# Optimization experiments

Hardware: AMD Instinct MI355X
Metric: run time of the kernel (lower is better)

The kernel has to match this reference:

```python
import jax, jax.numpy as jnp
import numpy as np

N, C, D, S = 512, 128, 16, 10
IR_DIMS = (1, 3, 5, 7)      # 0e, 1o, 2e, 3o
MUL1, MUL2, MUL3 = 1, 3, 7  # symmetric tensor-product path counts per order
INV_SQRT_C = 1.0 / np.sqrt(C).astype(np.float32)


def setup_inputs() -> dict:
    key = jax.random.key(0)
    ks = jax.random.split(key, 20)
    inp = {
        "node_feats": jax.random.normal(ks[0], (N, C, D), jnp.float32),
        "node_specie": jax.random.randint(ks[1], (N,), 0, S, jnp.int32),
    }
    # U basis tensors (stand-ins for e3nn reduced symmetric tensor product basis):
    # shape (D,)*order + (num_paths, ir_dim)
    for i, di in enumerate(IR_DIMS):
        inp[f"u1_{i}"] = jax.random.normal(ks[2 + i], (D, MUL1, di), jnp.float32) * 0.1
        inp[f"u2_{i}"] = jax.random.normal(ks[6 + i], (D, D, MUL2, di), jnp.float32) * 0.1
        inp[f"u3_{i}"] = jax.random.normal(ks[10 + i], (D, D, D, MUL3, di), jnp.float32) * 0.1
    # species-conditioned weights, init stddev mul**-0.5 (gradient_normalization='element')
    inp["w1"] = jax.random.normal(ks[14], (4, S, MUL1, C), jnp.float32) * MUL1 ** -0.5
    inp["w2"] = jax.random.normal(ks[15], (4, S, MUL2, C), jnp.float32) * MUL2 ** -0.5
    inp["w3"] = jax.random.normal(ks[16], (4, S, MUL3, C), jnp.float32) * MUL3 ** -0.5
    # e3nn Linear weights per output irrep: (C_in, C_out)
    inp["wlin"] = jax.random.normal(ks[17], (4, C, C), jnp.float32)
    return inp


def _product_basis(x, node_specie, u1s, u2s, u3s, w1, w2, w3, wlin):
    # x: (N, C, D). Recursive MACE symmetric contraction, vectorized over nodes.
    outs = []
    for i in range(4):  # loop over the 4 output irreps (fixed, structurally distinct)
        w3i = w3[i][node_specie]  # (N, MUL3, C) species gather
        w2i = w2[i][node_specie]  # (N, MUL2, C)
        w1i = w1[i][node_specie]  # (N, MUL1, C)
        # order 3: einsum('abjki,kc,cj->cabi', u3, w, x) per node
        a = jnp.einsum('nkc,ncj->njkc', w3i, x)               # (N, D, MUL3, C)
        out = jnp.einsum('abjki,njkc->ncabi', u3s[i], a)      # (N, C, D, D, di)
        # order 2 contribution, then contract one feature axis with x
        out = out + jnp.einsum('abki,nkc->ncabi', u2s[i], w2i)
        out = jnp.einsum('ncaji,ncj->ncai', out, x)           # (N, C, D, di)
        # order 1 contribution, then final contraction with x
        out = out + jnp.einsum('aki,nkc->ncai', u1s[i], w1i)
        out = jnp.einsum('ncji,ncj->nci', out, x)             # (N, C, di)
        # axis_to_mul + e3nn Linear (channel mixing per irrep, 1/sqrt(fan_in))
        y = jnp.einsum('nci,cf->nfi', out, wlin[i]) * INV_SQRT_C
        outs.append(y.reshape(y.shape[0], -1))
    return jnp.concatenate(outs, axis=-1)  # (N, C * sum(IR_DIMS)) = (N, 2048)


def reference(node_feats, node_specie, u1_0, u1_1, u1_2, u1_3,
              u2_0, u2_1, u2_2, u2_3, u3_0, u3_1, u3_2, u3_3,
              w1, w2, w3, wlin):
    return _product_basis(node_feats, node_specie,
                          (u1_0, u1_1, u1_2, u1_3),
                          (u2_0, u2_1, u2_2, u2_3),
                          (u3_0, u3_1, u3_2, u3_3),
                          w1, w2, w3, wlin)
```

## Files before the change

### kernel.cpp

```cpp
#include <hip/hip_runtime.h>

#define N_NODES 512
#define C_CH    128
#define S_SPEC  10
#define KT      50
#define NT      11

typedef _Float16 h8 __attribute__((ext_vector_type(8)));
typedef float f32x4 __attribute__((ext_vector_type(4)));

__device__ h8 g_Bf[KT * NT * 64];
__device__ h8 g_Wf[128 * 64];

__device__ __forceinline__ void o_to_iri(int o, int& ir, int& i) {
  if (o >= 9)      { ir = 3; i = o - 9; }
  else if (o >= 4) { ir = 2; i = o - 4; }
  else if (o >= 1) { ir = 1; i = o - 1; }
  else             { ir = 0; i = 0; }
}

__device__ int octet_desc(int Q) {
  if (Q < 172) {
    int q = Q;
    for (int a = 0; a < 16; ++a)
      for (int b = a; b < 16; ++b) {
        int no = (b < 8) ? 2 : 1;
        if (q < no) {
          int jb = (no == 1) ? 1 : q;
          return a | (b << 5) | (jb << 10);
        }
        q -= no;
      }
  } else if (Q < 196) {
    int q = Q - 172;
    for (int a = 0; a < 16; ++a) {
      int no = (a < 8) ? 2 : 1;
      if (q < no) {
        int jb = (no == 1) ? 1 : q;
        return a | (16 << 5) | (jb << 10);
      }
      q -= no;
    }
  } else if (Q < 198) {
    return 16 | (16 << 5) | ((Q - 196) << 10);
  }
  return 17 | (17 << 5);
}

__global__ void build_all(const float* __restrict__ u1_0, const float* __restrict__ u1_1,
                          const float* __restrict__ u1_2, const float* __restrict__ u1_3,
                          const float* __restrict__ u2_0, const float* __restrict__ u2_1,
                          const float* __restrict__ u2_2, const float* __restrict__ u2_3,
                          const float* __restrict__ u3_0, const float* __restrict__ u3_1,
                          const float* __restrict__ u3_2, const float* __restrict__ u3_3,
                          const float* __restrict__ wlin) {
  const int bid = blockIdx.x;
  const int dis[4] = {1, 3, 5, 7};
  if (bid < 320) {
    int kt, nt;
    if (bid < 301)      { kt = bid / 7; nt = bid % 7; }
    else if (bid < 319) { int e = bid - 301; kt = 43 + e / 3; nt = 7 + e % 3; }
    else                { kt = 49; nt = 10; }

    const int l = threadIdx.x;
    const int o = l & 15;
    int ir, ii; o_to_iri(o, ir, ii);
    const int di = dis[ir];
    const float* u1s[4] = {u1_0, u1_1, u1_2, u1_3};
    const float* u2s[4] = {u2_0, u2_1, u2_2, u2_3};
    const float* u3s[4] = {u3_0, u3_1, u3_2, u3_3};

    const int rt = octet_desc(kt * 4 + (l >> 4));
    const int oA = rt & 31, oB = (rt >> 5) & 31, j0 = ((rt >> 10) & 1) * 8;

    h8 v;
#pragma unroll
    for (int i = 0; i < 8; ++i) {
      const int j = j0 + i;
      float val = 0.f;
      if (oA < 16 && oB < 16) {
        if (j >= oB) {
          const float* u = u3s[ir];
          int a = oA, b = oB;
          int P[6][3] = {{a,b,j},{a,j,b},{b,a,j},{b,j,a},{j,a,b},{j,b,a}};
          for (int p = 0; p < 6; ++p) {
            bool dup = false;
            for (int r = 0; r < p; ++r)
              if (P[r][0] == P[p][0] && P[r][1] == P[p][1] && P[r][2] == P[p][2]) { dup = true; break; }
            if (!dup)
              val += u[(((P[p][0] * 16 + P[p][1]) * 16 + P[p][2]) * 7 + nt) * di + ii];
          }
        }
      } else if (oA < 16 && oB == 16) {
        if (j >= oA) {
          const int k2 = nt - 7;
          const float* u = u2s[ir];
          val = u[((oA * 16 + j) * 3 + k2) * di + ii];
          if (j != oA) val += u[((j * 16 + oA) * 3 + k2) * di + ii];
        }
      } else if (oA == 16) {
        val = u1s[ir][j * di + ii];
      }
      v[i] = (_Float16)val;
    }
    g_Bf[((size_t)kt * NT + nt) * 64 + l] = v;
  } else {
    const int id = (bid - 320) * 64 + threadIdx.x;
    const int l = id & 63, ks = (id >> 6) & 15, mt = id >> 10;
    const int f = mt * 16 + (l & 15);
    const float inv = 0.08838834764831845f;
    h8 v;
#pragma unroll
    for (int i = 0; i < 8; ++i) {
      const int k = ks * 32 + (l >> 4) * 8 + i;
      const int ir = k >> 7, cc = k & 127;
      v[i] = (_Float16)(wlin[((size_t)ir * C_CH + cc) * C_CH + f] * inv);
    }
    g_Wf[(mt * 16 + ks) * 64 + l] = v;
  }
}


#define MFMA16(A, B, C) __builtin_amdgcn_mfma_f32_16x16x32_f16(A, B, C, 0, 0, 0)

__global__ __launch_bounds__(512, 1) void eqp_mm(
    const float* __restrict__ x, const int* __restrict__ specie,
    const float* __restrict__ w1, const float* __restrict__ w2,
    const float* __restrict__ w3, float* __restrict__ out) {
  __shared__ __align__(16) char bs[2][70 * 1024];
  __shared__ float xT[2][128][18];
  __shared__ int rtab[KT * 4];

  const int t = threadIdx.x;
  const int l = t & 63;
  const int w = t >> 6;
  const int g = l >> 4;
  const int n0 = blockIdx.x * 2;

  {
    const int p = t >> 8, c = (t >> 1) & 127, half = t & 1;
    const float* xp = x + ((size_t)(n0 + p) * C_CH + c) * 16 + half * 8;
    const float4 v0 = *(const float4*)xp, v1 = *(const float4*)(xp + 4);
    float* row = &xT[p][c][half * 8];
    row[0] = v0.x; row[1] = v0.y; row[2] = v0.z; row[3] = v0.w;
    row[4] = v1.x; row[5] = v1.y; row[6] = v1.z; row[7] = v1.w;
    if (half == 1) { xT[p][c][16] = 1.f; xT[p][c][17] = 0.f; }
    if (t < KT * 4) rtab[t] = octet_desc(t);
  }

  const int ch = w * 16 + (l & 15);
  const int s0 = specie[n0], s1 = specie[n0 + 1];

  auto packh = [](float4 u, float4 v) {
    h8 r;
    r[0] = (_Float16)u.x; r[1] = (_Float16)u.y; r[2] = (_Float16)u.z; r[3] = (_Float16)u.w;
    r[4] = (_Float16)v.x; r[5] = (_Float16)v.y; r[6] = (_Float16)v.z; r[7] = (_Float16)v.w;
    return r;
  };
  h8 xh0l, xh0h, xh1l, xh1h;
  {
    const float4* p0 = (const float4*)(x + ((size_t)n0 * C_CH + ch) * 16);
    xh0l = packh(p0[0], p0[1]); xh0h = packh(p0[2], p0[3]);
    const float4* p1 = (const float4*)(x + ((size_t)(n0 + 1) * C_CH + ch) * 16);
    xh1l = packh(p1[0], p1[1]); xh1h = packh(p1[2], p1[3]);
  }

  f32x4 acc[2][NT];
#pragma unroll
  for (int p = 0; p < 2; ++p)
#pragma unroll
    for (int i = 0; i < NT; ++i) acc[p][i] = (f32x4){0.f, 0.f, 0.f, 0.f};

  h8 tv[9]; int dst[9];

  auto issue = [&](int ck) {
    const int f0 = ck * 70;
    const int nf = (ck < 4) ? 70 : 40;
#pragma unroll
    for (int slot = 0; slot < 9; ++slot) {
      const int r = slot * 8 + w;
      const bool ok = r < nf;
      const int fi = f0 + r;
      int kt, nt;
      if (fi < 301)      { kt = fi / 7;  nt = fi % 7; }
      else if (fi < 319) { kt = 43 + (fi - 301) / 3; nt = 7 + (fi - 301) % 3; }
      else               { kt = 49; nt = 10; }
      dst[slot] = ok ? r : -1;
      if (ok) tv[slot] = g_Bf[((size_t)kt * NT + nt) * 64 + l];
    }
  };
  auto wr = [&](char* buf) {
#pragma unroll
    for (int slot = 0; slot < 9; ++slot)
      if (dst[slot] >= 0) *(h8*)&buf[(size_t)dst[slot] * 1024 + (size_t)l * 16] = tv[slot];
  };

#define BRD(i) (*(const h8*)&buf[(size_t)(fb2 + (i)) * 1024 + (size_t)l * 16])

  auto consume = [&](int ck, const char* buf) {
    const int cs = ck * 10;
    int fb2 = 0;
#pragma unroll
    for (int tt = 0; tt < 10; ++tt) {
      const int kt = cs + tt;
      const int rt_ = rtab[kt * 4 + g];
      const int oA_ = rt_ & 31, oB_ = (rt_ >> 5) & 31, jb_ = (rt_ >> 10) & 1;
      const float xab0 = xT[0][ch][oA_] * xT[0][ch][oB_];
      const float xab1 = xT[1][ch][oA_] * xT[1][ch][oB_];
      const _Float16 hm0 = (_Float16)xab0, hm1 = (_Float16)xab1;
      const h8 m0 = {hm0, hm0, hm0, hm0, hm0, hm0, hm0, hm0};
      const h8 m1 = {hm1, hm1, hm1, hm1, hm1, hm1, hm1, hm1};
      const h8 af0 = m0 * (jb_ ? xh0h : xh0l);
      const h8 af1 = m1 * (jb_ ? xh1h : xh1l);
      if (kt < 43) {
        h8 b0 = BRD(0), b1 = BRD(1), b2 = BRD(2), b3 = BRD(3), b4 = BRD(4), b5 = BRD(5), b6 = BRD(6);
        acc[0][0] = MFMA16(af0, b0, acc[0][0]); acc[1][0] = MFMA16(af1, b0, acc[1][0]);
        acc[0][1] = MFMA16(af0, b1, acc[0][1]); acc[1][1] = MFMA16(af1, b1, acc[1][1]);
        acc[0][2] = MFMA16(af0, b2, acc[0][2]); acc[1][2] = MFMA16(af1, b2, acc[1][2]);
        acc[0][3] = MFMA16(af0, b3, acc[0][3]); acc[1][3] = MFMA16(af1, b3, acc[1][3]);
        acc[0][4] = MFMA16(af0, b4, acc[0][4]); acc[1][4] = MFMA16(af1, b4, acc[1][4]);
        acc[0][5] = MFMA16(af0, b5, acc[0][5]); acc[1][5] = MFMA16(af1, b5, acc[1][5]);
        acc[0][6] = MFMA16(af0, b6, acc[0][6]); acc[1][6] = MFMA16(af1, b6, acc[1][6]);
        fb2 += 7;
      } else if (kt < 49) {
        h8 b0 = BRD(0), b1 = BRD(1), b2 = BRD(2);
        acc[0][7] = MFMA16(af0, b0, acc[0][7]); acc[1][7] = MFMA16(af1, b0, acc[1][7]);
        acc[0][8] = MFMA16(af0, b1, acc[0][8]); acc[1][8] = MFMA16(af1, b1, acc[1][8]);
        acc[0][9] = MFMA16(af0, b2, acc[0][9]); acc[1][9] = MFMA16(af1, b2, acc[1][9]);
        fb2 += 3;
      } else {
        h8 b0 = BRD(0);
        acc[0][10] = MFMA16(af0, b0, acc[0][10]); acc[1][10] = MFMA16(af1, b0, acc[1][10]);
        fb2 += 1;
      }
    }
  };

  issue(0);
  __syncthreads();
  wr(bs[0]);
  __syncthreads();
#pragma unroll 1
  for (int ck = 0; ck < 5; ++ck) {
    if (ck < 4) issue(ck + 1);
    consume(ck, bs[ck & 1]);
    if (ck < 4) {
      wr(bs[(ck & 1) ^ 1]);
      __syncthreads();
    }
  }
  __syncthreads();

  _Float16* Ef = (_Float16*)&bs[0][0];
  {
    float4 z4 = {0.f, 0.f, 0.f, 0.f};
    float4* zp = (float4*)&bs[0][0];
    zp[t] = z4; zp[t + 512] = z4; zp[t + 1024] = z4; zp[t + 1536] = z4;
  }
  __syncthreads();
  {
    const int o = l & 15;
    int ir, ii; o_to_iri(o, ir, ii); (void)ii;
    const int cb = w * 16 + g * 4;
#pragma unroll
    for (int p = 0; p < 2; ++p) {
      const int sp = p ? s1 : s0;
      float tot[4] = {0.f, 0.f, 0.f, 0.f};
#pragma unroll
      for (int k = 0; k < 7; ++k) {
        const float4 wv = *(const float4*)(w3 + ((size_t)(ir * S_SPEC + sp) * 7 + k) * C_CH + cb);
        tot[0] = fmaf(wv.x, acc[p][k][0], tot[0]);
        tot[1] = fmaf(wv.y, acc[p][k][1], tot[1]);
        tot[2] = fmaf(wv.z, acc[p][k][2], tot[2]);
        tot[3] = fmaf(wv.w, acc[p][k][3], tot[3]);
      }
#pragma unroll
      for (int k = 0; k < 3; ++k) {
        const float4 wv = *(const float4*)(w2 + ((size_t)(ir * S_SPEC + sp) * 3 + k) * C_CH + cb);
        tot[0] = fmaf(wv.x, acc[p][7 + k][0], tot[0]);
        tot[1] = fmaf(wv.y, acc[p][7 + k][1], tot[1]);
        tot[2] = fmaf(wv.z, acc[p][7 + k][2], tot[2]);
        tot[3] = fmaf(wv.w, acc[p][7 + k][3], tot[3]);
      }
      {
        const float4 wv = *(const float4*)(w1 + (size_t)(ir * S_SPEC + sp) * C_CH + cb);
        tot[0] = fmaf(wv.x, acc[p][10][0], tot[0]);
        tot[1] = fmaf(wv.y, acc[p][10][1], tot[1]);
        tot[2] = fmaf(wv.z, acc[p][10][2], tot[2]);
        tot[3] = fmaf(wv.w, acc[p][10][3], tot[3]);
      }
#pragma unroll
      for (int r = 0; r < 4; ++r) {
        const int k = ir * 128 + cb + r;
        Ef[((((size_t)p * 16 + (k >> 5)) * 4 + ((k >> 3) & 3)) * 16 + o) * 8 + (k & 7)] =
            (_Float16)tot[r];
      }
    }
  }
  __syncthreads();

  {
    f32x4 D0 = {0.f, 0.f, 0.f, 0.f}, D1 = {0.f, 0.f, 0.f, 0.f};
#pragma unroll
    for (int ks = 0; ks < 16; ++ks) {
      const h8 aw = g_Wf[(w * 16 + ks) * 64 + l];
      const h8 b0 = *(const h8*)&Ef[(((size_t)0 * 16 + ks) * 4 + (l >> 4)) * 128 + (size_t)(l & 15) * 8];
      const h8 b1 = *(const h8*)&Ef[(((size_t)1 * 16 + ks) * 4 + (l >> 4)) * 128 + (size_t)(l & 15) * 8];
      D0 = MFMA16(aw, b0, D0);
      D1 = MFMA16(aw, b1, D1);
    }
    const int o = l & 15;
    int ir, ii; o_to_iri(o, ir, ii);
    const int dis[4]  = {1, 3, 5, 7};
    const int ooff[4] = {0, 128, 512, 1152};
#pragma unroll
    for (int p = 0; p < 2; ++p) {
      const f32x4 D = p ? D1 : D0;
      const size_t base = (size_t)(n0 + p) * 2048 + ooff[ir] + ii;
#pragma unroll
      for (int r = 0; r < 4; ++r) {
        const int f = w * 16 + (l >> 4) * 4 + r;
        out[base + (size_t)f * dis[ir]] = D[r];
      }
    }
  }
}


extern "C" void kernel_launch(void* const* d_in, const int* in_sizes, int n_in,
                              void* d_out, int out_size, void* d_ws, size_t ws_size,
                              hipStream_t stream) {
  const float* x      = (const float*)d_in[0];
  const int*   specie = (const int*)d_in[1];

  const float *u1s[4], *u2s[4], *u3s[4];
  if (in_sizes[3] == 768) {
    for (int i = 0; i < 4; ++i) {
      u1s[i] = (const float*)d_in[2 + 3 * i];
      u2s[i] = (const float*)d_in[3 + 3 * i];
      u3s[i] = (const float*)d_in[4 + 3 * i];
    }
  } else {
    for (int i = 0; i < 4; ++i) {
      u1s[i] = (const float*)d_in[2 + i];
      u2s[i] = (const float*)d_in[6 + i];
      u3s[i] = (const float*)d_in[10 + i];
    }
  }
  const float* w1   = (const float*)d_in[14];
  const float* w2   = (const float*)d_in[15];
  const float* w3   = (const float*)d_in[16];
  const float* wlin = (const float*)d_in[17];
  float* out = (float*)d_out;
  (void)d_ws; (void)ws_size; (void)out_size; (void)n_in;

  build_all<<<448, 64, 0, stream>>>(
      u1s[0], u1s[1], u1s[2], u1s[3],
      u2s[0], u2s[1], u2s[2], u2s[3],
      u3s[0], u3s[1], u3s[2], u3s[3], wlin);
  eqp_mm<<<N_NODES / 2, 512, 0, stream>>>(x, specie, w1, w2, w3, out);
}
```

Baseline: 62.55 us.

## Split K-dimension across two blocks and move channel-mixing GEMM to separate kernel

The main contraction kernel now splits its 50 K-tiles across two grid blocks (split-K), writing partial per-node contraction results to workspace. A new finalize kernel sums the partials and performs the Linear channel-mixing MFMA GEMM per node. Staging chunks shrink from 10 to 4 K-tiles, which cuts LDS per block so more blocks can be resident and the grid doubles from 256 blocks. This costs an extra kernel launch, a global round trip for the partials and a more complex tile-index computation in the issue loop.

```diff
diff --git a/kernel.cpp b/kernel.cpp
--- a/kernel.cpp
+++ b/kernel.cpp
@@ -11,6 +11,9 @@
 
 __device__ h8 g_Bf[KT * NT * 64];
 __device__ h8 g_Wf[128 * 64];
+
+__device__ __forceinline__ int fc_of(int kt)  { return kt < 43 ? 7 : (kt < 49 ? 3 : 1); }
+__device__ __forceinline__ int ntb_of(int kt) { return kt < 43 ? 0 : (kt < 49 ? 7 : 10); }
 
 __device__ __forceinline__ void o_to_iri(int o, int& ir, int& i) {
   if (o >= 9)      { ir = 3; i = o - 9; }
@@ -126,8 +129,8 @@
 __global__ __launch_bounds__(512, 1) void eqp_mm(
     const float* __restrict__ x, const int* __restrict__ specie,
     const float* __restrict__ w1, const float* __restrict__ w2,
-    const float* __restrict__ w3, float* __restrict__ out) {
-  __shared__ __align__(16) char bs[2][70 * 1024];
+    const float* __restrict__ w3, float* __restrict__ ws, int nsp) {
+  __shared__ __align__(16) char bs[2][28 * 1024];
   __shared__ float xT[2][128][18];
   __shared__ int rtab[KT * 4];
 
@@ -136,6 +139,7 @@
   const int w = t >> 6;
   const int g = l >> 4;
   const int n0 = blockIdx.x * 2;
+  const int ksp = blockIdx.y;
 
   {
     const int p = t >> 8, c = (t >> 1) & 127, half = t & 1;
@@ -171,37 +175,39 @@
 #pragma unroll
     for (int i = 0; i < NT; ++i) acc[p][i] = (f32x4){0.f, 0.f, 0.f, 0.f};
 
-  h8 tv[9]; int dst[9];
-
-  auto issue = [&](int ck) {
-    const int f0 = ck * 70;
-    const int nf = (ck < 4) ? 70 : 40;
-#pragma unroll
-    for (int slot = 0; slot < 9; ++slot) {
-      const int r = slot * 8 + w;
-      const bool ok = r < nf;
-      const int fi = f0 + r;
-      int kt, nt;
-      if (fi < 301)      { kt = fi / 7;  nt = fi % 7; }
-      else if (fi < 319) { kt = 43 + (fi - 301) / 3; nt = 7 + (fi - 301) % 3; }
-      else               { kt = 49; nt = 10; }
-      dst[slot] = ok ? r : -1;
-      if (ok) tv[slot] = g_Bf[((size_t)kt * NT + nt) * 64 + l];
+  const int T0   = (nsp == 2) ? ksp * 25 : 0;
+  const int tEnd = (nsp == 2) ? T0 + 25 : KT;
+  const int nck  = (tEnd - T0 + 3) / 4;
+
+  h8 tv[4]; int dst[4];
+
+  auto issue = [&](int cs) {
+    int nf = 0;
+#pragma unroll
+    for (int tt = 0; tt < 4; ++tt) if (cs + tt < tEnd) nf += fc_of(cs + tt);
+#pragma unroll
+    for (int slot = 0; slot < 4; ++slot) {
+      const int fi = slot * 8 + w;
+      const bool ok = fi < nf;
+      int kt = cs, rem = fi;
+      if (ok) { while (rem >= fc_of(kt)) { rem -= fc_of(kt); ++kt; } }
+      dst[slot] = ok ? fi : -1;
+      if (ok) tv[slot] = g_Bf[((size_t)kt * NT + (ntb_of(kt) + rem)) * 64 + l];
     }
   };
   auto wr = [&](char* buf) {
 #pragma unroll
-    for (int slot = 0; slot < 9; ++slot)
+    for (int slot = 0; slot < 4; ++slot)
       if (dst[slot] >= 0) *(h8*)&buf[(size_t)dst[slot] * 1024 + (size_t)l * 16] = tv[slot];
   };
 
 #define BRD(i) (*(const h8*)&buf[(size_t)(fb2 + (i)) * 1024 + (size_t)l * 16])
 
-  auto consume = [&](int ck, const char* buf) {
-    const int cs = ck * 10;
+  auto consume = [&](int cs, const char* buf) {
     int fb2 = 0;
 #pragma unroll
-    for (int tt = 0; tt < 10; ++tt) {
+    for (int tt = 0; tt < 4; ++tt) {
+      if (cs + tt >= tEnd) continue;
       const int kt = cs + tt;
       const int rt_ = rtab[kt * 4 + g];
       const int oA_ = rt_ & 31, oB_ = (rt_ >> 5) & 31, jb_ = (rt_ >> 10) & 1;
@@ -236,28 +242,21 @@
     }
   };
 
-  issue(0);
+  issue(T0);
   __syncthreads();
   wr(bs[0]);
   __syncthreads();
 #pragma unroll 1
-  for (int ck = 0; ck < 5; ++ck) {
-    if (ck < 4) issue(ck + 1);
-    consume(ck, bs[ck & 1]);
-    if (ck < 4) {
+  for (int ck = 0; ck < nck; ++ck) {
+    const int cs = T0 + ck * 4;
+    if (ck + 1 < nck) issue(cs + 4);
+    consume(cs, bs[ck & 1]);
+    if (ck + 1 < nck) {
       wr(bs[(ck & 1) ^ 1]);
       __syncthreads();
     }
   }
-  __syncthreads();
-
-  _Float16* Ef = (_Float16*)&bs[0][0];
-  {
-    float4 z4 = {0.f, 0.f, 0.f, 0.f};
-    float4* zp = (float4*)&bs[0][0];
-    zp[t] = z4; zp[t + 512] = z4; zp[t + 1024] = z4; zp[t + 1536] = z4;
-  }
-  __syncthreads();
+
   {
     const int o = l & 15;
     int ir, ii; o_to_iri(o, ir, ii); (void)ii;
@@ -289,39 +288,73 @@
         tot[2] = fmaf(wv.z, acc[p][10][2], tot[2]);
         tot[3] = fmaf(wv.w, acc[p][10][3], tot[3]);
       }
+      float4 st = {tot[0], tot[1], tot[2], tot[3]};
+      *(float4*)(ws + (((size_t)ksp * N_NODES + (n0 + p)) * 16 + o) * C_CH + cb) = st;
+    }
+  }
+}
+
+
+__global__ __launch_bounds__(256) void eqp_fin(
+    const float* __restrict__ ws, float* __restrict__ out, int nsp) {
+  __shared__ _Float16 Ef[8192];
+  const int t = threadIdx.x;
+  const int l = t & 63;
+  const int w = t >> 6;
+  const int n = blockIdx.x;
+
+  {
+    float4* z = (float4*)Ef;
+    z[t] = (float4){0.f, 0.f, 0.f, 0.f};
+    z[t + 256] = (float4){0.f, 0.f, 0.f, 0.f};
+    z[t + 512] = (float4){0.f, 0.f, 0.f, 0.f};
+    z[t + 768] = (float4){0.f, 0.f, 0.f, 0.f};
+  }
+  __syncthreads();
+
+  {
+    const float4* p0 = (const float4*)(ws + (size_t)n * 2048);
+    const float4* p1 = (const float4*)(ws + ((size_t)N_NODES + n) * 2048);
+#pragma unroll
+    for (int q = 0; q < 2; ++q) {
+      const int off = t + q * 256;
+      float4 a = p0[off];
+      if (nsp == 2) {
+        const float4 b = p1[off];
+        a.x += b.x; a.y += b.y; a.z += b.z; a.w += b.w;
+      }
+      const int o = off >> 5;
+      const int cbase = (off & 31) * 4;
+      int ir, ii; o_to_iri(o, ir, ii); (void)ii;
+      const float av[4] = {a.x, a.y, a.z, a.w};
 #pragma unroll
       for (int r = 0; r < 4; ++r) {
-        const int k = ir * 128 + cb + r;
-        Ef[((((size_t)p * 16 + (k >> 5)) * 4 + ((k >> 3) & 3)) * 16 + o) * 8 + (k & 7)] =
-            (_Float16)tot[r];
+        const int k = ir * 128 + cbase + r;
+        Ef[((((k >> 5) * 4) + ((k >> 3) & 3)) * 16 + o) * 8 + (k & 7)] = (_Float16)av[r];
       }
     }
   }
   __syncthreads();
 
-  {
-    f32x4 D0 = {0.f, 0.f, 0.f, 0.f}, D1 = {0.f, 0.f, 0.f, 0.f};
+  const int dis[4]  = {1, 3, 5, 7};
+  const int ooff[4] = {0, 128, 512, 1152};
+#pragma unroll
+  for (int mi = 0; mi < 2; ++mi) {
+    const int mt = w + mi * 4;
+    f32x4 D = {0.f, 0.f, 0.f, 0.f};
 #pragma unroll
     for (int ks = 0; ks < 16; ++ks) {
-      const h8 aw = g_Wf[(w * 16 + ks) * 64 + l];
-      const h8 b0 = *(const h8*)&Ef[(((size_t)0 * 16 + ks) * 4 + (l >> 4)) * 128 + (size_t)(l & 15) * 8];
-      const h8 b1 = *(const h8*)&Ef[(((size_t)1 * 16 + ks) * 4 + (l >> 4)) * 128 + (size_t)(l & 15) * 8];
-      D0 = MFMA16(aw, b0, D0);
-      D1 = MFMA16(aw, b1, D1);
+      const h8 aw = g_Wf[(mt * 16 + ks) * 64 + l];
+      const h8 b = *(const h8*)&Ef[((ks * 4 + (l >> 4)) * 16 + (l & 15)) * 8];
+      D = MFMA16(aw, b, D);
     }
     const int o = l & 15;
     int ir, ii; o_to_iri(o, ir, ii);
-    const int dis[4]  = {1, 3, 5, 7};
-    const int ooff[4] = {0, 128, 512, 1152};
-#pragma unroll
-    for (int p = 0; p < 2; ++p) {
-      const f32x4 D = p ? D1 : D0;
-      const size_t base = (size_t)(n0 + p) * 2048 + ooff[ir] + ii;
-#pragma unroll
-      for (int r = 0; r < 4; ++r) {
-        const int f = w * 16 + (l >> 4) * 4 + r;
-        out[base + (size_t)f * dis[ir]] = D[r];
-      }
+    const size_t base = (size_t)n * 2048 + ooff[ir] + ii;
+#pragma unroll
+    for (int r = 0; r < 4; ++r) {
+      const int f = mt * 16 + (l >> 4) * 4 + r;
+      out[base + (size_t)f * dis[ir]] = D[r];
     }
   }
 }
@@ -352,11 +385,16 @@
   const float* w3   = (const float*)d_in[16];
   const float* wlin = (const float*)d_in[17];
   float* out = (float*)d_out;
-  (void)d_ws; (void)ws_size; (void)out_size; (void)n_in;
+  float* ws  = (float*)d_ws;
+  (void)out_size; (void)n_in;
+
+  const size_t need2 = 2ull * N_NODES * 2048 * sizeof(float);
+  const int nsp = (ws_size >= need2) ? 2 : 1;
 
   build_all<<<448, 64, 0, stream>>>(
       u1s[0], u1s[1], u1s[2], u1s[3],
       u2s[0], u2s[1], u2s[2], u2s[3],
       u3s[0], u3s[1], u3s[2], u3s[3], wlin);
-  eqp_mm<<<N_NODES / 2, 512, 0, stream>>>(x, specie, w1, w2, w3, out);
-}
+  eqp_mm<<<dim3(N_NODES / 2, nsp), 512, 0, stream>>>(x, specie, w1, w2, w3, ws, nsp);
+  eqp_fin<<<N_NODES, 256, 0, stream>>>(ws, out, nsp);
+}
```

Result: slower. 94.24 us (+50.7%).
